# Optimization experiments

Measured on AMD Instinct MI355X. Metric: run time of the kernel, lower is better.

The kernel has to match this reference:

```python
import jax, jax.numpy as jnp
import numpy as np

D = 128        # feature_dims
ITERS = 2      # update_iters
B, R = 8, 256  # n segments (proteins), residues per segment
NEG_SLOPE = 0.1

def leaky(x):
    return jax.nn.leaky_relu(x, NEG_SLOPE)

def setup_inputs() -> dict:
    key = jax.random.key(0)
    ks = jax.random.split(key, 13)
    def w(k, shape):
        fan_in = shape[0]
        return jax.random.normal(k, shape, jnp.float32) / np.sqrt(fan_in)
    return {
        "fresidues": jax.random.normal(ks[0], (B, R, 20), jnp.float32),
        "coordinates": jax.random.normal(ks[1], (B, R, 3), jnp.float32) * 10.0,
        "W_emb": w(ks[2], (20, D)),                    # res_embedding (no bias)
        "W_e1": w(ks[3], (2 * D + 1, D)),              # linear_e layer 1
        "b_e1": jnp.zeros((D,), jnp.float32),
        "W_e2": w(ks[4], (D, D)),                      # linear_e layer 2
        "b_e2": jnp.zeros((D,), jnp.float32),
        "W_inf": w(ks[5], (D, 1)),                     # linear_inf gate
        "b_inf": jnp.zeros((1,), jnp.float32),
        "W_h1": w(ks[6], (2 * D, D)),                  # linear_h layer 1
        "b_h1": jnp.zeros((D,), jnp.float32),
        "W_h2": w(ks[7], (D, D)),                      # linear_h layer 2
        "b_h2": jnp.zeros((D,), jnp.float32),
    }

def reference(fresidues, coordinates, W_emb, W_e1, b_e1, W_e2, b_e2,
              W_inf, b_inf, W_h1, b_h1, W_h2, b_h2):
    # h: [B,R,D]
    h = leaky(fresidues @ W_emb)
    # pairwise squared distances: [B,R,R,1], constant across iterations
    d2 = jnp.sum(jnp.square(coordinates[:, :, None, :] - coordinates[:, None, :, :]),
                 axis=-1, keepdims=True)
    # mask out self-edges (1 - eye): [1,R,R,1]
    mask = (1.0 - jnp.eye(R, dtype=h.dtype))[None, :, :, None]
    # split edge-MLP first-layer weights to avoid materializing the [B,R,R,2D+1] concat:
    # m_input = cat([h_i, h_j, d2]) @ W_e1  ==  h_i@W_i + h_j@W_j + d2*w_d
    W_i, W_j, w_d = W_e1[:D], W_e1[D:2 * D], W_e1[2 * D]
    for _ in range(ITERS):
        ti = h @ W_i                                   # [B,R,D] receiver part
        tj = h @ W_j                                   # [B,R,D] sender part
        pre = ti[:, :, None, :] + tj[:, None, :, :] + d2 * w_d + b_e1  # [B,R,R,D]
        m = leaky(leaky(pre) @ W_e2 + b_e2)            # [B,R,R,D]
        e = jax.nn.sigmoid(m @ W_inf + b_inf) * mask   # [B,R,R,1]
        m_pre = jnp.sum(m * e, axis=2)                 # sum over senders j -> [B,R,D]
        hm = jnp.concatenate([h, m_pre], axis=-1)      # [B,R,2D]
        h = (leaky(hm @ W_h1 + b_h1) @ W_h2 + b_h2) + h
    return h

if __name__ == "__main__":
    out = reference(**setup_inputs())
    print(out.shape, out.dtype)
```

## Files before the change

### kernel.cpp

```cpp
#include <hip/hip_runtime.h>

typedef unsigned short ushort_t;
typedef __attribute__((ext_vector_type(8))) short shortx8;
typedef __attribute__((ext_vector_type(4))) float floatx4;
typedef __attribute__((ext_vector_type(2))) float floatx2;

#define NS 0.1f

__device__ __forceinline__ ushort_t f2bf_rne(float f) {
  union { float f; unsigned int u; } v; v.f = f;
  unsigned int r = v.u + 0x7FFFu + ((v.u >> 16) & 1u);
  return (ushort_t)(r >> 16);
}
__device__ __forceinline__ unsigned int pk2bf(float a, float b) {
  union { float f; unsigned int u; } x, y; x.f = a; y.f = b;
  return __builtin_amdgcn_perm(y.u + 0x8000u, x.u + 0x8000u, 0x07060302u);
}
__device__ __forceinline__ unsigned int cvtpk_bf16(float a, float b) {
  unsigned int r;
  asm("v_cvt_pk_bf16_f32 %0, %1, %2" : "=v"(r) : "v"(a), "v"(b));
  return r;
}
__device__ __forceinline__ ushort_t f2bf_rhu(float f) {
  union { float f; unsigned int u; } v; v.f = f;
  return (ushort_t)((v.u + 0x8000u) >> 16);
}
__device__ __forceinline__ float lk(float x) { return fmaxf(x, NS * x); }
__device__ __forceinline__ floatx2 lk2(floatx2 v) {
  return __builtin_elementwise_max(v, v * (floatx2){NS, NS});
}

__device__ __forceinline__ float row16_sum(float x) {
  int t;
  t = __builtin_amdgcn_update_dpp(0, __builtin_bit_cast(int, x), 0x128, 0xF, 0xF, true);
  x += __builtin_bit_cast(float, t);
  t = __builtin_amdgcn_update_dpp(0, __builtin_bit_cast(int, x), 0x124, 0xF, 0xF, true);
  x += __builtin_bit_cast(float, t);
  t = __builtin_amdgcn_update_dpp(0, __builtin_bit_cast(int, x), 0x4E, 0xF, 0xF, true);
  x += __builtin_bit_cast(float, t);
  t = __builtin_amdgcn_update_dpp(0, __builtin_bit_cast(int, x), 0xB1, 0xF, 0xF, true);
  x += __builtin_bit_cast(float, t);
  return x;
}

__global__ __launch_bounds__(256) void prep_w(
    const float* __restrict__ W_e1, const float* __restrict__ W_e2,
    const float* __restrict__ W_h1, const float* __restrict__ W_h2,
    ushort_t* __restrict__ wijf, ushort_t* __restrict__ we2f,
    ushort_t* __restrict__ wh1f, ushort_t* __restrict__ wh2f) {
  int e = blockIdx.x * 256 + threadIdx.x;
  int which, le;
  if (e < 32768) { which = 0; le = e; }
  else if (e < 49152) { which = 1; le = e - 32768; }
  else if (e < 81920) { which = 2; le = e - 49152; }
  else { which = 3; le = e - 81920; }
  const int NT = (which == 0) ? 16 : 8;
  int f = le >> 3, j = le & 7;
  int lane = f & 63, ft = f >> 6;
  int t = ft % NT, s = ft / NT;
  int n = t * 16 + (lane & 15), k = s * 32 + (lane >> 4) * 8 + j;
  float v; ushort_t* d;
  if (which == 0) { v = (n < 128) ? W_e1[k * 128 + n] : W_e1[(128 + k) * 128 + (n - 128)]; d = wijf; }
  else if (which == 1) { v = W_e2[k * 128 + n]; d = we2f; }
  else if (which == 2) { v = W_h1[k * 128 + n]; d = wh1f; }
  else { v = W_h2[k * 128 + n]; d = wh2f; }
  d[le] = f2bf_rne(v);
}

__device__ __forceinline__ void proj_store(float v, int m, int n,
                                           float* __restrict__ ti, float* __restrict__ tjf) {
  if (n < 128) {
    ti[(size_t)m * 128 + n] = v;
  } else {
    int k = n - 128, b = m >> 8, j = m & 255;
    int s = k >> 5, lg2 = (k >> 3) & 3, j8 = k & 7;
    tjf[((((size_t)(b * 4 + s)) * 256 + j) * 4 + lg2) * 8 + j8] = v;
  }
}

__global__ __launch_bounds__(256) void h0_proj(
    const float* __restrict__ fres, const float* __restrict__ Wemb,
    const ushort_t* __restrict__ wijf, float* __restrict__ h_out,
    float* __restrict__ ti, float* __restrict__ tjf) {
  const int m0 = blockIdx.x * 8;
  const int tid = threadIdx.x;
  const int w = tid >> 6, lane = tid & 63, l16 = lane & 15, lg = lane >> 4;
  __shared__ __align__(16) ushort_t sH[16][136];
  {
    const int row = tid >> 5, c0 = (tid & 31) * 4;
    const float* fr = fres + (size_t)(m0 + row) * 20;
    float a[4] = {0, 0, 0, 0};
    for (int k = 0; k < 20; ++k) {
      float fv = fr[k];
      float4 w0 = *(const float4*)(Wemb + k * 128 + c0);
      a[0] += fv * w0.x; a[1] += fv * w0.y; a[2] += fv * w0.z; a[3] += fv * w0.w;
    }
#pragma unroll
    for (int x = 0; x < 4; ++x) a[x] = lk(a[x]);
    float* ho = h_out + (size_t)(m0 + row) * 128 + c0;
    *(float4*)ho = (float4){a[0], a[1], a[2], a[3]};
    unsigned int* sh = (unsigned int*)&sH[row][c0];
    sh[0] = pk2bf(a[0], a[1]); sh[1] = pk2bf(a[2], a[3]);
  }
  __syncthreads();
  floatx4 ap[4];
#pragma unroll
  for (int q = 0; q < 4; ++q) ap[q] = (floatx4){0.f, 0.f, 0.f, 0.f};
  const shortx8* Wp = (const shortx8*)wijf;
#pragma unroll
  for (int s = 0; s < 4; ++s) {
    shortx8 af = *(const shortx8*)&sH[l16][s * 32 + lg * 8];
#pragma unroll
    for (int q = 0; q < 4; ++q)
      ap[q] = __builtin_amdgcn_mfma_f32_16x16x32_bf16(af, Wp[(s * 16 + 4 * w + q) * 64 + lane], ap[q], 0, 0, 0);
  }
#pragma unroll
  for (int q = 0; q < 4; ++q) {
    const int n = (4 * w + q) * 16 + l16;
#pragma unroll
    for (int r = 0; r < 4; ++r) {
      const int rl = lg * 4 + r;
      if (rl < 8) proj_store(ap[q][r], m0 + rl, n, ti, tjf);
    }
  }
}

__global__ __launch_bounds__(256, 2) void edge_kernel(
    const float* __restrict__ ti, const float* __restrict__ tjf,
    const float* __restrict__ coords, const ushort_t* __restrict__ we2f,
    const float* __restrict__ W_e1, const float* __restrict__ b_e1,
    const float* __restrict__ b_e2, const float* __restrict__ W_inf,
    const float* __restrict__ b_inf, float* __restrict__ mp0, float* __restrict__ mp1) {
  const int blk = blockIdx.x;
  const int b = blk & 7;
  const int ch = (blk >> 3) & 1;
  const int ip = blk >> 4;
  const int i0 = ip * 2;
  const int tid = threadIdx.x;
  const int w = tid >> 6, lane = tid & 63, l16 = lane & 15, lg = lane >> 4;

  __shared__ __align__(16) ushort_t sW[16384];
  __shared__ __align__(16) float sTiP[2][128];
  __shared__ __align__(16) float sWd[128];
  __shared__ __align__(16) float sD2[2][128];
  __shared__ __align__(16) float sMp[2][4][128];

  {
    const int wbase = tid & ~63;
#pragma unroll
    for (int r = 0; r < 8; ++r) {
      const ushort_t* g = we2f + (size_t)(r * 256 + tid) * 8;
      ushort_t* l = (ushort_t*)sW + (size_t)(r * 256 + wbase) * 8;
      __builtin_amdgcn_global_load_lds(g, l, 16, 0, 0);
    }
  }
  if (tid < 128) {
    sTiP[0][tid] = ti[(size_t)(b * 256 + i0) * 128 + tid] + b_e1[tid];
    sWd[tid] = W_e1[256 * 128 + tid];
  } else {
    const int t2 = tid - 128;
    sTiP[1][t2] = ti[(size_t)(b * 256 + i0 + 1) * 128 + t2] + b_e1[t2];
  }
  {
    const int ii = tid >> 7, jj = tid & 127;
    const int iv = i0 + ii, jv = ch * 128 + jj;
    float dx = coords[(size_t)(b * 256 + iv) * 3 + 0] - coords[(size_t)(b * 256 + jv) * 3 + 0];
    float dy = coords[(size_t)(b * 256 + iv) * 3 + 1] - coords[(size_t)(b * 256 + jv) * 3 + 1];
    float dz = coords[(size_t)(b * 256 + iv) * 3 + 2] - coords[(size_t)(b * 256 + jv) * 3 + 2];
    sD2[ii][jj] = dx * dx + dy * dy + dz * dz;
  }

  floatx4 acc[2][2][8];
#pragma unroll
  for (int t = 0; t < 8; ++t) {
    float bv = b_e2[t * 16 + l16];
    floatx4 v = (floatx4){bv, bv, bv, bv};
    acc[0][0][t] = v; acc[0][1][t] = v; acc[1][0][t] = v; acc[1][1][t] = v;
  }
  __syncthreads();

  float d2a[2][2];
#pragma unroll
  for (int ii = 0; ii < 2; ++ii)
#pragma unroll
    for (int c = 0; c < 2; ++c)
      d2a[ii][c] = sD2[ii][c * 64 + w * 16 + l16];
  const shortx8* sWf = (const shortx8*)sW;

#pragma unroll
  for (int s = 0; s < 4; ++s) {
    const int k0 = s * 32 + lg * 8;
    floatx2 w2[4];
#pragma unroll
    for (int x = 0; x < 4; ++x) w2[x] = *(const floatx2*)&sWd[k0 + 2 * x];
    shortx8 af[2][2];
#pragma unroll
    for (int c = 0; c < 2; ++c) {
      const int jr = ch * 128 + c * 64 + w * 16 + l16;
      const float* tb = tjf + (((size_t)(b * 4 + s) * 256 + jr) * 4 + lg) * 8;
      float4 t0 = *(const float4*)tb;
      float4 t1 = *(const float4*)(tb + 4);
#pragma unroll
      for (int ii = 0; ii < 2; ++ii) {
        floatx2 p0 = *(const floatx2*)&sTiP[ii][k0 + 0];
        floatx2 p1 = *(const floatx2*)&sTiP[ii][k0 + 2];
        floatx2 p2v = *(const floatx2*)&sTiP[ii][k0 + 4];
        floatx2 p3 = *(const floatx2*)&sTiP[ii][k0 + 6];
        const floatx2 d2v = (floatx2){d2a[ii][c], d2a[ii][c]};
        floatx2 l0 = lk2((floatx2){t0.x, t0.y} + (p0 + d2v * w2[0]));
        floatx2 l1 = lk2((floatx2){t0.z, t0.w} + (p1 + d2v * w2[1]));
        floatx2 l2 = lk2((floatx2){t1.x, t1.y} + (p2v + d2v * w2[2]));
        floatx2 l3 = lk2((floatx2){t1.z, t1.w} + (p3 + d2v * w2[3]));
        union { shortx8 s8; unsigned int u[4]; } A;
        A.u[0] = cvtpk_bf16(l0.x, l0.y); A.u[1] = cvtpk_bf16(l1.x, l1.y);
        A.u[2] = cvtpk_bf16(l2.x, l2.y); A.u[3] = cvtpk_bf16(l3.x, l3.y);
        af[ii][c] = A.s8;
      }
    }
#pragma unroll
    for (int tg = 0; tg < 2; ++tg) {
      shortx8 b0 = sWf[(s * 8 + tg * 4 + 0) * 64 + lane];
      shortx8 b1 = sWf[(s * 8 + tg * 4 + 1) * 64 + lane];
      shortx8 b2 = sWf[(s * 8 + tg * 4 + 2) * 64 + lane];
      shortx8 b3 = sWf[(s * 8 + tg * 4 + 3) * 64 + lane];
      __builtin_amdgcn_s_setprio(1);
#pragma unroll
      for (int ii = 0; ii < 2; ++ii)
#pragma unroll
        for (int c = 0; c < 2; ++c) {
          acc[ii][c][tg * 4 + 0] = __builtin_amdgcn_mfma_f32_16x16x32_bf16(af[ii][c], b0, acc[ii][c][tg * 4 + 0], 0, 0, 0);
          acc[ii][c][tg * 4 + 1] = __builtin_amdgcn_mfma_f32_16x16x32_bf16(af[ii][c], b1, acc[ii][c][tg * 4 + 1], 0, 0, 0);
          acc[ii][c][tg * 4 + 2] = __builtin_amdgcn_mfma_f32_16x16x32_bf16(af[ii][c], b2, acc[ii][c][tg * 4 + 2], 0, 0, 0);
          acc[ii][c][tg * 4 + 3] = __builtin_amdgcn_mfma_f32_16x16x32_bf16(af[ii][c], b3, acc[ii][c][tg * 4 + 3], 0, 0, 0);
        }
      __builtin_amdgcn_s_setprio(0);
    }
  }

  float winfv[8];
#pragma unroll
  for (int t = 0; t < 8; ++t) winfv[t] = W_inf[t * 16 + l16];
  const float binf = b_inf[0];
#pragma unroll
  for (int ii = 0; ii < 2; ++ii) {
    const int i = i0 + ii;
    float mpacc[8];
#pragma unroll
    for (int t = 0; t < 8; ++t) mpacc[t] = 0.f;
#pragma unroll
    for (int c = 0; c < 2; ++c) {
#pragma unroll
      for (int t = 0; t < 8; ++t) {
        floatx2 v0 = lk2((floatx2){acc[ii][c][t][0], acc[ii][c][t][1]});
        floatx2 v1 = lk2((floatx2){acc[ii][c][t][2], acc[ii][c][t][3]});
        acc[ii][c][t][0] = v0.x; acc[ii][c][t][1] = v0.y;
        acc[ii][c][t][2] = v1.x; acc[ii][c][t][3] = v1.y;
      }
#pragma unroll
      for (int r = 0; r < 4; ++r) {
        float sum = 0.f;
#pragma unroll
        for (int t = 0; t < 8; ++t) sum += acc[ii][c][t][r] * winfv[t];
        sum = row16_sum(sum);
        const int jg = ch * 128 + c * 64 + w * 16 + lg * 4 + r;
        float x = sum + binf;
        float e = __builtin_amdgcn_rcpf(1.f + __expf(-x));
        if (jg == i) e = 0.f;
#pragma unroll
        for (int t = 0; t < 8; ++t) mpacc[t] += acc[ii][c][t][r] * e;
      }
    }
#pragma unroll
    for (int t = 0; t < 8; ++t) {
      mpacc[t] += __shfl_xor(mpacc[t], 16);
      mpacc[t] += __shfl_xor(mpacc[t], 32);
    }
    if (lg == 0) {
#pragma unroll
      for (int t = 0; t < 8; ++t) sMp[ii][w][t * 16 + l16] = mpacc[t];
    }
  }
  __syncthreads();
  {
    const int ii = tid >> 7, col = tid & 127;
    float v = sMp[ii][0][col] + sMp[ii][1][col] + sMp[ii][2][col] + sMp[ii][3][col];
    float* mpo = ch ? mp1 : mp0;
    mpo[(size_t)(b * 256 + i0 + ii) * 128 + col] = v;
  }
}

__global__ __launch_bounds__(256) void node_kernel(
    const float* __restrict__ h_in, const float* __restrict__ mp0, const float* __restrict__ mp1,
    const ushort_t* __restrict__ wh1f, const float* __restrict__ b_h1,
    const ushort_t* __restrict__ wh2f, const float* __restrict__ b_h2,
    const ushort_t* __restrict__ wijf, float* __restrict__ h_out,
    float* __restrict__ ti, float* __restrict__ tjf, const int do_proj) {
  const int m0 = blockIdx.x * 8;
  const int tid = threadIdx.x;
  const int w = tid >> 6, lane = tid & 63, l16 = lane & 15, lg = lane >> 4;
  __shared__ __align__(16) ushort_t sA[16][264];
  __shared__ __align__(16) ushort_t sU[16][136];
  __shared__ __align__(16) ushort_t sHp[16][136];

  {
    const int row = tid >> 5, c0 = (tid & 31) * 8;
    unsigned int* dst = (unsigned int*)&sA[row][c0];
    if (c0 < 128) {
      const float* src = h_in + (size_t)(m0 + row) * 128 + c0;
#pragma unroll
      for (int x = 0; x < 4; ++x) dst[x] = pk2bf(src[2 * x], src[2 * x + 1]);
    } else {
      const float* s0 = mp0 + (size_t)(m0 + row) * 128 + (c0 - 128);
      const float* s1 = mp1 + (size_t)(m0 + row) * 128 + (c0 - 128);
#pragma unroll
      for (int x = 0; x < 4; ++x)
        dst[x] = pk2bf(s0[2 * x] + s1[2 * x], s0[2 * x + 1] + s1[2 * x + 1]);
    }
  }
  __syncthreads();
  floatx4 au[2];
#pragma unroll
  for (int q = 0; q < 2; ++q) { float bv = b_h1[(2 * w + q) * 16 + l16]; au[q] = (floatx4){bv, bv, bv, bv}; }
  const shortx8* W1 = (const shortx8*)wh1f;
#pragma unroll
  for (int s = 0; s < 8; ++s) {
    shortx8 af = *(const shortx8*)&sA[l16][s * 32 + lg * 8];
#pragma unroll
    for (int q = 0; q < 2; ++q)
      au[q] = __builtin_amdgcn_mfma_f32_16x16x32_bf16(af, W1[(s * 8 + 2 * w + q) * 64 + lane], au[q], 0, 0, 0);
  }
#pragma unroll
  for (int q = 0; q < 2; ++q)
#pragma unroll
    for (int r = 0; r < 4; ++r) {
      const int rl = lg * 4 + r;
      if (rl < 8) sU[rl][(2 * w + q) * 16 + l16] = f2bf_rhu(lk(au[q][r]));
    }
  __syncthreads();
  floatx4 ah[2];
#pragma unroll
  for (int q = 0; q < 2; ++q) { float bv = b_h2[(2 * w + q) * 16 + l16]; ah[q] = (floatx4){bv, bv, bv, bv}; }
  const shortx8* W2 = (const shortx8*)wh2f;
#pragma unroll
  for (int s = 0; s < 4; ++s) {
    shortx8 af = *(const shortx8*)&sU[l16][s * 32 + lg * 8];
#pragma unroll
    for (int q = 0; q < 2; ++q)
      ah[q] = __builtin_amdgcn_mfma_f32_16x16x32_bf16(af, W2[(s * 8 + 2 * w + q) * 64 + lane], ah[q], 0, 0, 0);
  }
#pragma unroll
  for (int q = 0; q < 2; ++q) {
    const int n = (2 * w + q) * 16 + l16;
#pragma unroll
    for (int r = 0; r < 4; ++r) {
      const int rl = lg * 4 + r;
      if (rl < 8) {
        const int m = m0 + rl;
        float v = ah[q][r] + h_in[(size_t)m * 128 + n];
        h_out[(size_t)m * 128 + n] = v;
        sHp[rl][n] = f2bf_rhu(v);
      }
    }
  }
  if (!do_proj) return;
  __syncthreads();
  floatx4 ap[4];
#pragma unroll
  for (int q = 0; q < 4; ++q) ap[q] = (floatx4){0.f, 0.f, 0.f, 0.f};
  const shortx8* Wp = (const shortx8*)wijf;
#pragma unroll
  for (int s = 0; s < 4; ++s) {
    shortx8 af = *(const shortx8*)&sHp[l16][s * 32 + lg * 8];
#pragma unroll
    for (int q = 0; q < 4; ++q)
      ap[q] = __builtin_amdgcn_mfma_f32_16x16x32_bf16(af, Wp[(s * 16 + 4 * w + q) * 64 + lane], ap[q], 0, 0, 0);
  }
#pragma unroll
  for (int q = 0; q < 4; ++q) {
    const int n = (4 * w + q) * 16 + l16;
#pragma unroll
    for (int r = 0; r < 4; ++r) {
      const int rl = lg * 4 + r;
      if (rl < 8) proj_store(ap[q][r], m0 + rl, n, ti, tjf);
    }
  }
}

extern "C" void kernel_launch(void* const* d_in, const int* in_sizes, int n_in,
                              void* d_out, int out_size, void* d_ws, size_t ws_size,
                              hipStream_t stream) {
  const float* fres   = (const float*)d_in[0];
  const float* coords = (const float*)d_in[1];
  const float* W_emb  = (const float*)d_in[2];
  const float* W_e1   = (const float*)d_in[3];
  const float* b_e1   = (const float*)d_in[4];
  const float* W_e2   = (const float*)d_in[5];
  const float* b_e2   = (const float*)d_in[6];
  const float* W_inf  = (const float*)d_in[7];
  const float* b_inf  = (const float*)d_in[8];
  const float* W_h1   = (const float*)d_in[9];
  const float* b_h1   = (const float*)d_in[10];
  const float* W_h2   = (const float*)d_in[11];
  const float* b_h2   = (const float*)d_in[12];
  float* out = (float*)d_out;

  char* ws = (char*)d_ws;
  float* hA  = (float*)(ws + (0 << 20));
  float* hB  = (float*)(ws + (1 << 20));
  float* tib = (float*)(ws + (2 << 20));
  float* tjf = (float*)(ws + (3 << 20));
  float* mp0 = (float*)(ws + (4 << 20));
  float* mp1 = (float*)(ws + (5 << 20));
  ushort_t* wijf = (ushort_t*)(ws + (6 << 20));
  ushort_t* we2f = wijf + 32768;
  ushort_t* wh1f = we2f + 16384;
  ushort_t* wh2f = wh1f + 32768;

  prep_w<<<384, 256, 0, stream>>>(W_e1, W_e2, W_h1, W_h2, wijf, we2f, wh1f, wh2f);
  h0_proj<<<256, 256, 0, stream>>>(fres, W_emb, wijf, hA, tib, tjf);

  edge_kernel<<<2048, 256, 0, stream>>>(tib, tjf, coords, we2f, W_e1, b_e1, b_e2, W_inf, b_inf, mp0, mp1);
  node_kernel<<<256, 256, 0, stream>>>(hA, mp0, mp1, wh1f, b_h1, wh2f, b_h2, wijf, hB, tib, tjf, 1);

  edge_kernel<<<2048, 256, 0, stream>>>(tib, tjf, coords, we2f, W_e1, b_e1, b_e2, W_inf, b_inf, mp0, mp1);
  node_kernel<<<256, 256, 0, stream>>>(hB, mp0, mp1, wh1f, b_h1, wh2f, b_h2, wijf, out, tib, tjf, 0);
}
```

Baseline: 163.8 us.

## Fuse edge and node kernels into one per-iteration kernel with full sender loop

Merges the edge message kernel and the node update kernel into a single kernel. Each block now loops over both sender halves itself, so the two partial message sums no longer go through global memory. The block then applies the node MLP and projection to its 2 receiver rows. Projection outputs are double-buffered so the next iteration's inputs are not overwritten while other blocks still read them. This removes two launches and the mp round trip. In exchange the grid is halved, and the node MLP runs MFMA tiles that are mostly padding (2 useful rows of 16), so node work per block is largely redundant.

```diff
diff --git a/kernel.cpp b/kernel.cpp
--- a/kernel.cpp
+++ b/kernel.cpp
@@ -125,16 +125,20 @@
   }
 }
 
-__global__ __launch_bounds__(256, 2) void edge_kernel(
-    const float* __restrict__ ti, const float* __restrict__ tjf,
+__global__ __launch_bounds__(256, 2) void edge_node(
+    const float* __restrict__ ti_in, const float* __restrict__ tjf_in,
     const float* __restrict__ coords, const ushort_t* __restrict__ we2f,
     const float* __restrict__ W_e1, const float* __restrict__ b_e1,
     const float* __restrict__ b_e2, const float* __restrict__ W_inf,
-    const float* __restrict__ b_inf, float* __restrict__ mp0, float* __restrict__ mp1) {
+    const float* __restrict__ b_inf,
+    const float* __restrict__ h_in, const ushort_t* __restrict__ wh1f,
+    const float* __restrict__ b_h1, const ushort_t* __restrict__ wh2f,
+    const float* __restrict__ b_h2, const ushort_t* __restrict__ wijf,
+    float* __restrict__ h_out, float* __restrict__ ti_out,
+    float* __restrict__ tjf_out, const int do_proj) {
   const int blk = blockIdx.x;
   const int b = blk & 7;
-  const int ch = (blk >> 3) & 1;
-  const int ip = blk >> 4;
+  const int ip = blk >> 3;
   const int i0 = ip * 2;
   const int tid = threadIdx.x;
   const int w = tid >> 6, lane = tid & 63, l16 = lane & 15, lg = lane >> 4;
@@ -142,8 +146,12 @@
   __shared__ __align__(16) ushort_t sW[16384];
   __shared__ __align__(16) float sTiP[2][128];
   __shared__ __align__(16) float sWd[128];
-  __shared__ __align__(16) float sD2[2][128];
+  __shared__ __align__(16) float sD2[2][256];
   __shared__ __align__(16) float sMp[2][4][128];
+  __shared__ __align__(16) float sMpF[2][128];
+  __shared__ __align__(16) ushort_t sA[16][264];
+  __shared__ __align__(16) ushort_t sU[16][136];
+  __shared__ __align__(16) ushort_t sHp[16][136];
 
   {
     const int wbase = tid & ~63;
@@ -155,166 +163,161 @@
     }
   }
   if (tid < 128) {
-    sTiP[0][tid] = ti[(size_t)(b * 256 + i0) * 128 + tid] + b_e1[tid];
+    sTiP[0][tid] = ti_in[(size_t)(b * 256 + i0) * 128 + tid] + b_e1[tid];
     sWd[tid] = W_e1[256 * 128 + tid];
   } else {
     const int t2 = tid - 128;
-    sTiP[1][t2] = ti[(size_t)(b * 256 + i0 + 1) * 128 + t2] + b_e1[t2];
-  }
-  {
-    const int ii = tid >> 7, jj = tid & 127;
-    const int iv = i0 + ii, jv = ch * 128 + jj;
+    sTiP[1][t2] = ti_in[(size_t)(b * 256 + i0 + 1) * 128 + t2] + b_e1[t2];
+  }
+#pragma unroll
+  for (int e = 0; e < 2; ++e) {
+    const int idx = e * 256 + tid;
+    const int ii = idx >> 8, jv = idx & 255;
+    const int iv = i0 + ii;
     float dx = coords[(size_t)(b * 256 + iv) * 3 + 0] - coords[(size_t)(b * 256 + jv) * 3 + 0];
     float dy = coords[(size_t)(b * 256 + iv) * 3 + 1] - coords[(size_t)(b * 256 + jv) * 3 + 1];
     float dz = coords[(size_t)(b * 256 + iv) * 3 + 2] - coords[(size_t)(b * 256 + jv) * 3 + 2];
-    sD2[ii][jj] = dx * dx + dy * dy + dz * dz;
-  }
-
-  floatx4 acc[2][2][8];
+    sD2[ii][jv] = dx * dx + dy * dy + dz * dz;
+  }
+
+  float bv8[8], winfv[8];
 #pragma unroll
   for (int t = 0; t < 8; ++t) {
-    float bv = b_e2[t * 16 + l16];
-    floatx4 v = (floatx4){bv, bv, bv, bv};
-    acc[0][0][t] = v; acc[0][1][t] = v; acc[1][0][t] = v; acc[1][1][t] = v;
-  }
-  __syncthreads();
-
-  float d2a[2][2];
-#pragma unroll
-  for (int ii = 0; ii < 2; ++ii)
-#pragma unroll
-    for (int c = 0; c < 2; ++c)
-      d2a[ii][c] = sD2[ii][c * 64 + w * 16 + l16];
+    bv8[t] = b_e2[t * 16 + l16];
+    winfv[t] = W_inf[t * 16 + l16];
+  }
+  const float binf = b_inf[0];
+  __syncthreads();
+
   const shortx8* sWf = (const shortx8*)sW;
 
-#pragma unroll
-  for (int s = 0; s < 4; ++s) {
-    const int k0 = s * 32 + lg * 8;
-    floatx2 w2[4];
-#pragma unroll
-    for (int x = 0; x < 4; ++x) w2[x] = *(const floatx2*)&sWd[k0 + 2 * x];
-    shortx8 af[2][2];
-#pragma unroll
-    for (int c = 0; c < 2; ++c) {
-      const int jr = ch * 128 + c * 64 + w * 16 + l16;
-      const float* tb = tjf + (((size_t)(b * 4 + s) * 256 + jr) * 4 + lg) * 8;
-      float4 t0 = *(const float4*)tb;
-      float4 t1 = *(const float4*)(tb + 4);
-#pragma unroll
-      for (int ii = 0; ii < 2; ++ii) {
-        floatx2 p0 = *(const floatx2*)&sTiP[ii][k0 + 0];
-        floatx2 p1 = *(const floatx2*)&sTiP[ii][k0 + 2];
-        floatx2 p2v = *(const floatx2*)&sTiP[ii][k0 + 4];
-        floatx2 p3 = *(const floatx2*)&sTiP[ii][k0 + 6];
-        const floatx2 d2v = (floatx2){d2a[ii][c], d2a[ii][c]};
-        floatx2 l0 = lk2((floatx2){t0.x, t0.y} + (p0 + d2v * w2[0]));
-        floatx2 l1 = lk2((floatx2){t0.z, t0.w} + (p1 + d2v * w2[1]));
-        floatx2 l2 = lk2((floatx2){t1.x, t1.y} + (p2v + d2v * w2[2]));
-        floatx2 l3 = lk2((floatx2){t1.z, t1.w} + (p3 + d2v * w2[3]));
-        union { shortx8 s8; unsigned int u[4]; } A;
-        A.u[0] = cvtpk_bf16(l0.x, l0.y); A.u[1] = cvtpk_bf16(l1.x, l1.y);
-        A.u[2] = cvtpk_bf16(l2.x, l2.y); A.u[3] = cvtpk_bf16(l3.x, l3.y);
-        af[ii][c] = A.s8;
-      }
-    }
-#pragma unroll
-    for (int tg = 0; tg < 2; ++tg) {
-      shortx8 b0 = sWf[(s * 8 + tg * 4 + 0) * 64 + lane];
-      shortx8 b1 = sWf[(s * 8 + tg * 4 + 1) * 64 + lane];
-      shortx8 b2 = sWf[(s * 8 + tg * 4 + 2) * 64 + lane];
-      shortx8 b3 = sWf[(s * 8 + tg * 4 + 3) * 64 + lane];
-      __builtin_amdgcn_s_setprio(1);
-#pragma unroll
-      for (int ii = 0; ii < 2; ++ii)
-#pragma unroll
-        for (int c = 0; c < 2; ++c) {
-          acc[ii][c][tg * 4 + 0] = __builtin_amdgcn_mfma_f32_16x16x32_bf16(af[ii][c], b0, acc[ii][c][tg * 4 + 0], 0, 0, 0);
-          acc[ii][c][tg * 4 + 1] = __builtin_amdgcn_mfma_f32_16x16x32_bf16(af[ii][c], b1, acc[ii][c][tg * 4 + 1], 0, 0, 0);
-          acc[ii][c][tg * 4 + 2] = __builtin_amdgcn_mfma_f32_16x16x32_bf16(af[ii][c], b2, acc[ii][c][tg * 4 + 2], 0, 0, 0);
-          acc[ii][c][tg * 4 + 3] = __builtin_amdgcn_mfma_f32_16x16x32_bf16(af[ii][c], b3, acc[ii][c][tg * 4 + 3], 0, 0, 0);
+  for (int ch = 0; ch < 2; ++ch) {
+    floatx4 acc[2][2][8];
+#pragma unroll
+    for (int t = 0; t < 8; ++t) {
+      floatx4 v = (floatx4){bv8[t], bv8[t], bv8[t], bv8[t]};
+      acc[0][0][t] = v; acc[0][1][t] = v; acc[1][0][t] = v; acc[1][1][t] = v;
+    }
+    float d2a[2][2];
+#pragma unroll
+    for (int ii = 0; ii < 2; ++ii)
+#pragma unroll
+      for (int c = 0; c < 2; ++c)
+        d2a[ii][c] = sD2[ii][ch * 128 + c * 64 + w * 16 + l16];
+
+#pragma unroll
+    for (int s = 0; s < 4; ++s) {
+      const int k0 = s * 32 + lg * 8;
+      floatx2 w2[4];
+#pragma unroll
+      for (int x = 0; x < 4; ++x) w2[x] = *(const floatx2*)&sWd[k0 + 2 * x];
+      shortx8 af[2][2];
+#pragma unroll
+      for (int c = 0; c < 2; ++c) {
+        const int jr = ch * 128 + c * 64 + w * 16 + l16;
+        const float* tb = tjf_in + (((size_t)(b * 4 + s) * 256 + jr) * 4 + lg) * 8;
+        float4 t0 = *(const float4*)tb;
+        float4 t1 = *(const float4*)(tb + 4);
+#pragma unroll
+        for (int ii = 0; ii < 2; ++ii) {
+          floatx2 p0 = *(const floatx2*)&sTiP[ii][k0 + 0];
+          floatx2 p1 = *(const floatx2*)&sTiP[ii][k0 + 2];
+          floatx2 p2v = *(const floatx2*)&sTiP[ii][k0 + 4];
+          floatx2 p3 = *(const floatx2*)&sTiP[ii][k0 + 6];
+          const floatx2 d2v = (floatx2){d2a[ii][c], d2a[ii][c]};
+          floatx2 l0 = lk2((floatx2){t0.x, t0.y} + (p0 + d2v * w2[0]));
+          floatx2 l1 = lk2((floatx2){t0.z, t0.w} + (p1 + d2v * w2[1]));
+          floatx2 l2 = lk2((floatx2){t1.x, t1.y} + (p2v + d2v * w2[2]));
+          floatx2 l3 = lk2((floatx2){t1.z, t1.w} + (p3 + d2v * w2[3]));
+          union { shortx8 s8; unsigned int u[4]; } A;
+          A.u[0] = cvtpk_bf16(l0.x, l0.y); A.u[1] = cvtpk_bf16(l1.x, l1.y);
+          A.u[2] = cvtpk_bf16(l2.x, l2.y); A.u[3] = cvtpk_bf16(l3.x, l3.y);
+          af[ii][c] = A.s8;
         }
-      __builtin_amdgcn_s_setprio(0);
-    }
-  }
-
-  float winfv[8];
-#pragma unroll
-  for (int t = 0; t < 8; ++t) winfv[t] = W_inf[t * 16 + l16];
-  const float binf = b_inf[0];
-#pragma unroll
-  for (int ii = 0; ii < 2; ++ii) {
-    const int i = i0 + ii;
-    float mpacc[8];
-#pragma unroll
-    for (int t = 0; t < 8; ++t) mpacc[t] = 0.f;
-#pragma unroll
-    for (int c = 0; c < 2; ++c) {
+      }
+#pragma unroll
+      for (int tg = 0; tg < 2; ++tg) {
+        shortx8 b0 = sWf[(s * 8 + tg * 4 + 0) * 64 + lane];
+        shortx8 b1 = sWf[(s * 8 + tg * 4 + 1) * 64 + lane];
+        shortx8 b2 = sWf[(s * 8 + tg * 4 + 2) * 64 + lane];
+        shortx8 b3 = sWf[(s * 8 + tg * 4 + 3) * 64 + lane];
+        __builtin_amdgcn_s_setprio(1);
+#pragma unroll
+        for (int ii = 0; ii < 2; ++ii)
+#pragma unroll
+          for (int c = 0; c < 2; ++c) {
+            acc[ii][c][tg * 4 + 0] = __builtin_amdgcn_mfma_f32_16x16x32_bf16(af[ii][c], b0, acc[ii][c][tg * 4 + 0], 0, 0, 0);
+            acc[ii][c][tg * 4 + 1] = __builtin_amdgcn_mfma_f32_16x16x32_bf16(af[ii][c], b1, acc[ii][c][tg * 4 + 1], 0, 0, 0);
+            acc[ii][c][tg * 4 + 2] = __builtin_amdgcn_mfma_f32_16x16x32_bf16(af[ii][c], b2, acc[ii][c][tg * 4 + 2], 0, 0, 0);
+            acc[ii][c][tg * 4 + 3] = __builtin_amdgcn_mfma_f32_16x16x32_bf16(af[ii][c], b3, acc[ii][c][tg * 4 + 3], 0, 0, 0);
+          }
+        __builtin_amdgcn_s_setprio(0);
+      }
+    }
+
+#pragma unroll
+    for (int ii = 0; ii < 2; ++ii) {
+      const int i = i0 + ii;
+      float mpacc[8];
+#pragma unroll
+      for (int t = 0; t < 8; ++t) mpacc[t] = 0.f;
+#pragma unroll
+      for (int c = 0; c < 2; ++c) {
+#pragma unroll
+        for (int t = 0; t < 8; ++t) {
+          floatx2 v0 = lk2((floatx2){acc[ii][c][t][0], acc[ii][c][t][1]});
+          floatx2 v1 = lk2((floatx2){acc[ii][c][t][2], acc[ii][c][t][3]});
+          acc[ii][c][t][0] = v0.x; acc[ii][c][t][1] = v0.y;
+          acc[ii][c][t][2] = v1.x; acc[ii][c][t][3] = v1.y;
+        }
+#pragma unroll
+        for (int r = 0; r < 4; ++r) {
+          float sum = 0.f;
+#pragma unroll
+          for (int t = 0; t < 8; ++t) sum += acc[ii][c][t][r] * winfv[t];
+          sum = row16_sum(sum);
+          const int jg = ch * 128 + c * 64 + w * 16 + lg * 4 + r;
+          float x = sum + binf;
+          float e = __builtin_amdgcn_rcpf(1.f + __expf(-x));
+          if (jg == i) e = 0.f;
+#pragma unroll
+          for (int t = 0; t < 8; ++t) mpacc[t] += acc[ii][c][t][r] * e;
+        }
+      }
 #pragma unroll
       for (int t = 0; t < 8; ++t) {
-        floatx2 v0 = lk2((floatx2){acc[ii][c][t][0], acc[ii][c][t][1]});
-        floatx2 v1 = lk2((floatx2){acc[ii][c][t][2], acc[ii][c][t][3]});
-        acc[ii][c][t][0] = v0.x; acc[ii][c][t][1] = v0.y;
-        acc[ii][c][t][2] = v1.x; acc[ii][c][t][3] = v1.y;
-      }
-#pragma unroll
-      for (int r = 0; r < 4; ++r) {
-        float sum = 0.f;
-#pragma unroll
-        for (int t = 0; t < 8; ++t) sum += acc[ii][c][t][r] * winfv[t];
-        sum = row16_sum(sum);
-        const int jg = ch * 128 + c * 64 + w * 16 + lg * 4 + r;
-        float x = sum + binf;
-        float e = __builtin_amdgcn_rcpf(1.f + __expf(-x));
-        if (jg == i) e = 0.f;
-#pragma unroll
-        for (int t = 0; t < 8; ++t) mpacc[t] += acc[ii][c][t][r] * e;
-      }
-    }
-#pragma unroll
-    for (int t = 0; t < 8; ++t) {
-      mpacc[t] += __shfl_xor(mpacc[t], 16);
-      mpacc[t] += __shfl_xor(mpacc[t], 32);
-    }
-    if (lg == 0) {
-#pragma unroll
-      for (int t = 0; t < 8; ++t) sMp[ii][w][t * 16 + l16] = mpacc[t];
+        mpacc[t] += __shfl_xor(mpacc[t], 16);
+        mpacc[t] += __shfl_xor(mpacc[t], 32);
+      }
+      if (lg == 0) {
+        if (ch == 0) {
+#pragma unroll
+          for (int t = 0; t < 8; ++t) sMp[ii][w][t * 16 + l16] = mpacc[t];
+        } else {
+#pragma unroll
+          for (int t = 0; t < 8; ++t) sMp[ii][w][t * 16 + l16] += mpacc[t];
+        }
+      }
     }
   }
   __syncthreads();
   {
     const int ii = tid >> 7, col = tid & 127;
-    float v = sMp[ii][0][col] + sMp[ii][1][col] + sMp[ii][2][col] + sMp[ii][3][col];
-    float* mpo = ch ? mp1 : mp0;
-    mpo[(size_t)(b * 256 + i0 + ii) * 128 + col] = v;
-  }
-}
-
-__global__ __launch_bounds__(256) void node_kernel(
-    const float* __restrict__ h_in, const float* __restrict__ mp0, const float* __restrict__ mp1,
-    const ushort_t* __restrict__ wh1f, const float* __restrict__ b_h1,
-    const ushort_t* __restrict__ wh2f, const float* __restrict__ b_h2,
-    const ushort_t* __restrict__ wijf, float* __restrict__ h_out,
-    float* __restrict__ ti, float* __restrict__ tjf, const int do_proj) {
-  const int m0 = blockIdx.x * 8;
-  const int tid = threadIdx.x;
-  const int w = tid >> 6, lane = tid & 63, l16 = lane & 15, lg = lane >> 4;
-  __shared__ __align__(16) ushort_t sA[16][264];
-  __shared__ __align__(16) ushort_t sU[16][136];
-  __shared__ __align__(16) ushort_t sHp[16][136];
-
-  {
+    sMpF[ii][col] = sMp[ii][0][col] + sMp[ii][1][col] + sMp[ii][2][col] + sMp[ii][3][col];
+  }
+  __syncthreads();
+
+  if (tid < 64) {
     const int row = tid >> 5, c0 = (tid & 31) * 8;
     unsigned int* dst = (unsigned int*)&sA[row][c0];
     if (c0 < 128) {
-      const float* src = h_in + (size_t)(m0 + row) * 128 + c0;
+      const float* src = h_in + (size_t)(b * 256 + i0 + row) * 128 + c0;
 #pragma unroll
       for (int x = 0; x < 4; ++x) dst[x] = pk2bf(src[2 * x], src[2 * x + 1]);
     } else {
-      const float* s0 = mp0 + (size_t)(m0 + row) * 128 + (c0 - 128);
-      const float* s1 = mp1 + (size_t)(m0 + row) * 128 + (c0 - 128);
-#pragma unroll
-      for (int x = 0; x < 4; ++x)
-        dst[x] = pk2bf(s0[2 * x] + s1[2 * x], s0[2 * x + 1] + s1[2 * x + 1]);
+      const float* s0 = &sMpF[row][c0 - 128];
+#pragma unroll
+      for (int x = 0; x < 4; ++x) dst[x] = pk2bf(s0[2 * x], s0[2 * x + 1]);
     }
   }
   __syncthreads();
@@ -334,7 +337,7 @@
 #pragma unroll
     for (int r = 0; r < 4; ++r) {
       const int rl = lg * 4 + r;
-      if (rl < 8) sU[rl][(2 * w + q) * 16 + l16] = f2bf_rhu(lk(au[q][r]));
+      if (rl < 2) sU[rl][(2 * w + q) * 16 + l16] = f2bf_rhu(lk(au[q][r]));
     }
   __syncthreads();
   floatx4 ah[2];
@@ -354,10 +357,10 @@
 #pragma unroll
     for (int r = 0; r < 4; ++r) {
       const int rl = lg * 4 + r;
-      if (rl < 8) {
-        const int m = m0 + rl;
-        float v = ah[q][r] + h_in[(size_t)m * 128 + n];
-        h_out[(size_t)m * 128 + n] = v;
+      if (rl < 2) {
+        const size_t m = (size_t)(b * 256 + i0 + rl);
+        float v = ah[q][r] + h_in[m * 128 + n];
+        h_out[m * 128 + n] = v;
         sHp[rl][n] = f2bf_rhu(v);
       }
     }
@@ -381,7 +384,7 @@
 #pragma unroll
     for (int r = 0; r < 4; ++r) {
       const int rl = lg * 4 + r;
-      if (rl < 8) proj_store(ap[q][r], m0 + rl, n, ti, tjf);
+      if (rl < 2) proj_store(ap[q][r], b * 256 + i0 + rl, n, ti_out, tjf_out);
     }
   }
 }
@@ -405,23 +408,22 @@
   float* out = (float*)d_out;
 
   char* ws = (char*)d_ws;
-  float* hA  = (float*)(ws + (0 << 20));
-  float* hB  = (float*)(ws + (1 << 20));
-  float* tib = (float*)(ws + (2 << 20));
-  float* tjf = (float*)(ws + (3 << 20));
-  float* mp0 = (float*)(ws + (4 << 20));
-  float* mp1 = (float*)(ws + (5 << 20));
+  float* hA   = (float*)(ws + (0 << 20));
+  float* hB   = (float*)(ws + (1 << 20));
+  float* ti0  = (float*)(ws + (2 << 20));
+  float* tjf0 = (float*)(ws + (3 << 20));
+  float* ti1  = (float*)(ws + (4 << 20));
+  float* tjf1 = (float*)(ws + (5 << 20));
   ushort_t* wijf = (ushort_t*)(ws + (6 << 20));
   ushort_t* we2f = wijf + 32768;
   ushort_t* wh1f = we2f + 16384;
   ushort_t* wh2f = wh1f + 32768;
 
   prep_w<<<384, 256, 0, stream>>>(W_e1, W_e2, W_h1, W_h2, wijf, we2f, wh1f, wh2f);
-  h0_proj<<<256, 256, 0, stream>>>(fres, W_emb, wijf, hA, tib, tjf);
-
-  edge_kernel<<<2048, 256, 0, stream>>>(tib, tjf, coords, we2f, W_e1, b_e1, b_e2, W_inf, b_inf, mp0, mp1);
-  node_kernel<<<256, 256, 0, stream>>>(hA, mp0, mp1, wh1f, b_h1, wh2f, b_h2, wijf, hB, tib, tjf, 1);
-
-  edge_kernel<<<2048, 256, 0, stream>>>(tib, tjf, coords, we2f, W_e1, b_e1, b_e2, W_inf, b_inf, mp0, mp1);
-  node_kernel<<<256, 256, 0, stream>>>(hB, mp0, mp1, wh1f, b_h1, wh2f, b_h2, wijf, out, tib, tjf, 0);
-}
+  h0_proj<<<256, 256, 0, stream>>>(fres, W_emb, wijf, hA, ti0, tjf0);
+
+  edge_node<<<1024, 256, 0, stream>>>(ti0, tjf0, coords, we2f, W_e1, b_e1, b_e2, W_inf, b_inf,
+                                      hA, wh1f, b_h1, wh2f, b_h2, wijf, hB, ti1, tjf1, 1);
+  edge_node<<<1024, 256, 0, stream>>>(ti1, tjf1, coords, we2f, W_e1, b_e1, b_e2, W_inf, b_inf,
+                                      hB, wh1f, b_h1, wh2f, b_h2, wijf, out, ti0, tjf0, 0);
+}
```

Measured after the change: 177.3 us. 1.08x slower.
